# Optimization experiments

Measured on AMD Instinct MI355X. Metric: run time of the kernel, lower is better.

## Reference

```python
import jax, jax.numpy as jnp
import numpy as np
from jax import lax

KSIZE = 11
SIGMA_COLOR = 0.05
SIGMA_SPACE = 8.0
WEIGHT = (10.0, 35.0, 1.0, 10.0)

# --- fixed kernels (numpy, baked as constants) ---
_SOBEL_X = np.array([[-1, 0, 1], [-2, 0, 2], [-1, 0, 1]], np.float32).reshape(1, 1, 3, 3)
_SOBEL_Y = np.array([[1, 2, 1], [0, 0, 0], [-1, -2, -1]], np.float32).reshape(1, 1, 3, 3)

def _gaussian_window(size=11, sigma=1.5):
    g = np.exp(-((np.arange(size) - size // 2) ** 2) / (2.0 * sigma ** 2))
    g = g / g.sum()
    w = np.outer(g, g).astype(np.float32)
    return w.reshape(1, 1, size, size)

_SSIM_WIN = _gaussian_window()

# spatial weights for bilateral filter: gaussian over offset distance
_off = np.arange(KSIZE) - KSIZE // 2
_dy, _dx = np.meshgrid(_off, _off, indexing='ij')
_W_SPACE = np.exp(-(_dx ** 2 + _dy ** 2) / (2.0 * SIGMA_SPACE ** 2)).astype(np.float32).reshape(KSIZE * KSIZE, 1, 1)

def _conv2d(x, k, padding):
    return lax.conv_general_dilated(x, jnp.asarray(k), (1, 1), padding,
                                    dimension_numbers=('NCHW', 'OIHW', 'NCHW'))

def sobelxy(x):
    # ReflectionPad2d(1) then 3x3 sobel convs, |gx| + |gy|
    xp = jnp.pad(x, ((0, 0), (0, 0), (1, 1), (1, 1)), mode='reflect')
    gx = _conv2d(xp, _SOBEL_X, 'VALID')
    gy = _conv2d(xp, _SOBEL_Y, 'VALID')
    return jnp.abs(gx) + jnp.abs(gy)

def bilateral_filter(x):
    # x: [B,1,H,W]; reflect-pad, extract 11x11 patches, joint space*color weights
    p = KSIZE // 2
    xp = jnp.pad(x, ((0, 0), (0, 0), (p, p), (p, p)), mode='reflect')
    patches = lax.conv_general_dilated_patches(xp, (KSIZE, KSIZE), (1, 1), 'VALID',
                                               dimension_numbers=('NCHW', 'OIHW', 'NCHW'))
    # patches: [B, 121, H, W]; center pixel is x itself
    w_color = jnp.exp(-((patches - x) ** 2) / (2.0 * SIGMA_COLOR ** 2))
    w = w_color * jnp.asarray(_W_SPACE)[None]
    return (w * patches).sum(axis=1, keepdims=True) / w.sum(axis=1, keepdims=True)

def ssim(img1, img2):
    # standard pytorch-ssim: 11x11 gaussian window, zero-pad SAME, size_average mean
    C1, C2 = 0.01 ** 2, 0.03 ** 2
    pad = [(5, 5), (5, 5)]
    mu1 = _conv2d(img1, _SSIM_WIN, pad)
    mu2 = _conv2d(img2, _SSIM_WIN, pad)
    mu1_sq, mu2_sq, mu1_mu2 = mu1 * mu1, mu2 * mu2, mu1 * mu2
    sigma1_sq = _conv2d(img1 * img1, _SSIM_WIN, pad) - mu1_sq
    sigma2_sq = _conv2d(img2 * img2, _SSIM_WIN, pad) - mu2_sq
    sigma12 = _conv2d(img1 * img2, _SSIM_WIN, pad) - mu1_mu2
    ssim_map = ((2 * mu1_mu2 + C1) * (2 * sigma12 + C2)) / ((mu1_sq + mu2_sq + C1) * (sigma1_sq + sigma2_sq + C2))
    return ssim_map.mean()

def setup_inputs() -> dict:
    key = jax.random.key(0)
    k1, k2, k3 = jax.random.split(key, 3)
    B, H, W = 4, 480, 640
    return {
        'image_vis': jax.random.uniform(k1, (B, 3, H, W), jnp.float32),
        'image_ir': jax.random.uniform(k2, (B, 1, H, W), jnp.float32),
        'generate_img': jax.random.uniform(k3, (B, 1, H, W), jnp.float32),
    }

def reference(image_vis, image_ir, generate_img):
    image_y = image_vis[:, :1, :, :]
    x_in_max = jnp.maximum(image_y, image_ir)
    loss_in = jnp.abs(generate_img - x_in_max).mean()

    ir_grad = sobelxy(bilateral_filter(image_ir))
    y_grad = sobelxy(image_y)
    gen_grad = sobelxy(generate_img)
    x_grad_joint = jnp.maximum(y_grad, ir_grad)
    loss_grad = jnp.abs(gen_grad - x_grad_joint).mean()

    loss_tra = jnp.abs(generate_img - (image_ir + image_y) * 0.5).mean()

    loss_ssim = (1.0 - ssim(image_y, generate_img)) / 2 + (1.0 - ssim(image_ir, generate_img)) / 2

    loss_total = (WEIGHT[0] * loss_in + WEIGHT[1] * loss_grad
                  + WEIGHT[2] * loss_ssim + WEIGHT[3] * loss_tra)
    return (loss_total, loss_in, loss_grad, loss_ssim, loss_tra)
```

## Files before the change

kernel.cpp:

```cpp
#include <hip/hip_runtime.h>

#define IMG_H 480
#define IMG_W 640
#define IMG_B 4
#define HWSZ (IMG_H*IMG_W)
#define NPIX (IMG_B*HWSZ)
#define NBLK 4800

typedef float __attribute__((ext_vector_type(2))) f32x2;

constexpr float GW[11] = {
    0.00102838f, 0.00759878f, 0.03600077f, 0.10936067f, 0.21300555f,
    0.26601174f,
    0.21300555f, 0.10936067f, 0.03600077f, 0.00759878f, 0.00102838f};

constexpr float LG2WS[11] = {
    -0.28177637f, -0.18033688f, -0.10143950f, -0.04508422f, -0.01127106f,
    0.0f,
    -0.01127106f, -0.04508422f, -0.10143950f, -0.18033688f, -0.28177637f};
#define C_COLOR (-288.53900818f)

__device__ inline float fexp2(float x) {
#if __has_builtin(__builtin_amdgcn_exp2f)
    return __builtin_amdgcn_exp2f(x);
#else
    return exp2f(x);
#endif
}

__device__ inline int refl(int i, int n) {
    return i < 0 ? -i : (i >= n ? 2*n - 2 - i : i);
}

__device__ inline float sobel_abs(const float* __restrict__ p,
                                  int ym, int y0, int yp, int xm, int x0, int xp) {
    float a = p[ym*IMG_W+xm], b = p[ym*IMG_W+x0], c = p[ym*IMG_W+xp];
    float d = p[y0*IMG_W+xm],                      e = p[y0*IMG_W+xp];
    float f = p[yp*IMG_W+xm], g = p[yp*IMG_W+x0], h = p[yp*IMG_W+xp];
    float gx = (c + 2.f*e + h) - (a + 2.f*d + f);
    float gy = (a + 2.f*b + c) - (f + 2.f*g + h);
    return fabsf(gx) + fabsf(gy);
}

__global__ __launch_bounds__(256)
void bilateral_kernel(const float* __restrict__ ir, float* __restrict__ bf) {
    __shared__ __attribute__((aligned(16))) float tile[26][42];
    const int tx = threadIdx.x, ty = threadIdx.y;
    const int x0 = blockIdx.x*32, y0 = blockIdx.y*16, b = blockIdx.z;
    const float* src = ir + b*HWSZ;
    const int tid = ty*16 + tx;
    for (int i = tid; i < 26*42; i += 256) {
        int r = i / 42, c = i % 42;
        int gy = refl(y0 - 5 + r, IMG_H);
        int gx = refl(x0 - 5 + c, IMG_W);
        tile[r][c] = src[gy*IMG_W + gx];
    }
    __syncthreads();

    const int px = 2*tx;
    f32x2 cen = { tile[ty+5][px+5], tile[ty+5][px+6] };
    f32x2 num = {0.f, 0.f}, den = {0.f, 0.f};
    #pragma unroll
    for (int dy = 0; dy < 11; ++dy) {
        float w[12];
        #pragma unroll
        for (int k = 0; k < 6; ++k) {
            f32x2 p = *reinterpret_cast<const f32x2*>(&tile[ty+dy][px + 2*k]);
            w[2*k] = p.x; w[2*k+1] = p.y;
        }
        #pragma unroll
        for (int dx = 0; dx < 11; ++dx) {
            const float c2 = LG2WS[dy] + LG2WS[dx];
            f32x2 v = { w[dx], w[dx+1] };
            f32x2 d = v - cen;
            f32x2 arg = d*d*C_COLOR + c2;
            f32x2 wt;
            wt.x = fexp2(arg.x);
            wt.y = fexp2(arg.y);
            num += wt*v;
            den += wt;
        }
    }
    f32x2 res = num / den;
    *reinterpret_cast<f32x2*>(&bf[b*HWSZ + (y0+ty)*IMG_W + x0 + px]) = res;
}

__global__ __launch_bounds__(128)
void ssim_kernel(const float* __restrict__ vis, const float* __restrict__ ir,
                 const float* __restrict__ gen, float* __restrict__ parts) {
    __shared__ __attribute__((aligned(16))) float sy[18][42], si[18][42], sg[18][42];
    __shared__ __attribute__((aligned(16))) float hs[8][18][32];
    const int tx = threadIdx.x, ty = threadIdx.y;
    const int x0 = blockIdx.x*32, y0 = blockIdx.y*8, b = blockIdx.z;
    const int tid = ty*16 + tx;
    const int gid = blockIdx.x + 20*blockIdx.y + 1200*blockIdx.z;
    const float* py = vis + b*3*HWSZ;
    const float* pi = ir  + b*HWSZ;
    const float* pg = gen + b*HWSZ;

    for (int i = tid; i < 42*18; i += 128) {
        int r = i / 42, c = i % 42;
        int gy = y0 - 5 + r, gx = x0 - 5 + c;
        bool ok = (gy >= 0) & (gy < IMG_H) & (gx >= 0) & (gx < IMG_W);
        int idx = ok ? gy*IMG_W + gx : 0;
        float vy = ok ? py[idx] : 0.f;
        float vi = ok ? pi[idx] : 0.f;
        float vg = ok ? pg[idx] : 0.f;
        sy[r][c] = vy; si[r][c] = vi; sg[r][c] = vg;
    }
    __syncthreads();

    for (int i = tid; i < 18*16; i += 128) {
        int r = i / 16, c = 2*(i % 16);
        float wy[12], wi[12], wg[12];
        #pragma unroll
        for (int k = 0; k < 6; ++k) {
            f32x2 p0 = *reinterpret_cast<const f32x2*>(&sy[r][c + 2*k]);
            f32x2 p1 = *reinterpret_cast<const f32x2*>(&si[r][c + 2*k]);
            f32x2 p2 = *reinterpret_cast<const f32x2*>(&sg[r][c + 2*k]);
            wy[2*k] = p0.x; wy[2*k+1] = p0.y;
            wi[2*k] = p1.x; wi[2*k+1] = p1.y;
            wg[2*k] = p2.x; wg[2*k+1] = p2.y;
        }
        f32x2 a0={0,0},a1={0,0},a2={0,0},a3={0,0},a4={0,0},a5={0,0},a6={0,0},a7={0,0};
        #pragma unroll
        for (int dx = 0; dx < 11; ++dx) {
            const float g = GW[dx];
            f32x2 vy = { wy[dx], wy[dx+1] };
            f32x2 vi = { wi[dx], wi[dx+1] };
            f32x2 vg = { wg[dx], wg[dx+1] };
            f32x2 gy = g*vy, gi = g*vi, gg = g*vg;
            a0 += gy;    a1 += gi;    a2 += gg;
            a3 += gy*vy; a4 += gi*vi; a5 += gg*vg;
            a6 += gy*vg; a7 += gi*vg;
        }
        *reinterpret_cast<f32x2*>(&hs[0][r][c]) = a0;
        *reinterpret_cast<f32x2*>(&hs[1][r][c]) = a1;
        *reinterpret_cast<f32x2*>(&hs[2][r][c]) = a2;
        *reinterpret_cast<f32x2*>(&hs[3][r][c]) = a3;
        *reinterpret_cast<f32x2*>(&hs[4][r][c]) = a4;
        *reinterpret_cast<f32x2*>(&hs[5][r][c]) = a5;
        *reinterpret_cast<f32x2*>(&hs[6][r][c]) = a6;
        *reinterpret_cast<f32x2*>(&hs[7][r][c]) = a7;
    }
    __syncthreads();

    const int px = 2*tx;
    f32x2 s[8];
    #pragma unroll
    for (int f = 0; f < 8; ++f) {
        f32x2 acc = {0.f, 0.f};
        #pragma unroll
        for (int dy = 0; dy < 11; ++dy)
            acc += GW[dy] * (*reinterpret_cast<const f32x2*>(&hs[f][ty+dy][px]));
        s[f] = acc;
    }
    const float C1 = 1e-4f, C2 = 9e-4f;
    f32x2 muY = s[0], muI = s[1], muG = s[2];
    f32x2 vY  = s[3] - muY*muY, vI = s[4] - muI*muI, vG = s[5] - muG*muG;
    f32x2 cYG = s[6] - muY*muG, cIG = s[7] - muI*muG;
    f32x2 ssimYG = ((2.f*muY*muG + C1)*(2.f*cYG + C2)) /
                   ((muY*muY + muG*muG + C1)*(vY + vG + C2));
    f32x2 ssimIG = ((2.f*muI*muG + C1)*(2.f*cIG + C2)) /
                   ((muI*muI + muG*muG + C1)*(vI + vG + C2));

    float v0 = ssimYG.x + ssimYG.y, v1 = ssimIG.x + ssimIG.y;
    #pragma unroll
    for (int off = 32; off > 0; off >>= 1) {
        v0 += __shfl_down(v0, off);
        v1 += __shfl_down(v1, off);
    }
    __shared__ float red[2][2];
    int lane = tid & 63, wv = tid >> 6;
    if (lane == 0) { red[0][wv] = v0; red[1][wv] = v1; }
    __syncthreads();
    if (tid == 0) {
        parts[3*NBLK + gid] = red[0][0] + red[0][1];
        parts[4*NBLK + gid] = red[1][0] + red[1][1];
    }
}

__global__ __launch_bounds__(256)
void grad_kernel(const float* __restrict__ vis, const float* __restrict__ ir,
                 const float* __restrict__ gen, const float* __restrict__ bf,
                 float* __restrict__ parts) {
    const int idx = blockIdx.x*256 + threadIdx.x;
    const int b = idx / HWSZ, rem = idx % HWSZ;
    const int y = rem / IMG_W, x = rem % IMG_W;
    const float* py = vis + b*3*HWSZ;
    const float* pi = ir  + b*HWSZ;
    const float* pg = gen + b*HWSZ;
    const float* pb = bf  + b*HWSZ;

    const int ym = (y == 0) ? 1 : y-1, yp = (y == IMG_H-1) ? IMG_H-2 : y+1;
    const int xm = (x == 0) ? 1 : x-1, xp = (x == IMG_W-1) ? IMG_W-2 : x+1;

    float yg = sobel_abs(py, ym, y, yp, xm, x, xp);
    float ig = sobel_abs(pb, ym, y, yp, xm, x, xp);
    float gg = sobel_abs(pg, ym, y, yp, xm, x, xp);
    float tgrad = fabsf(gg - fmaxf(yg, ig));

    float cy = py[y*IMG_W+x], ci = pi[y*IMG_W+x], cg = pg[y*IMG_W+x];
    float tin  = fabsf(cg - fmaxf(cy, ci));
    float ttra = fabsf(cg - 0.5f*(ci + cy));

    float v0 = tin, v1 = tgrad, v2 = ttra;
    #pragma unroll
    for (int off = 32; off > 0; off >>= 1) {
        v0 += __shfl_down(v0, off);
        v1 += __shfl_down(v1, off);
        v2 += __shfl_down(v2, off);
    }
    __shared__ float red[3][4];
    int lane = threadIdx.x & 63, wv = threadIdx.x >> 6;
    if (lane == 0) { red[0][wv] = v0; red[1][wv] = v1; red[2][wv] = v2; }
    __syncthreads();
    if (threadIdx.x == 0) {
        parts[0*NBLK + blockIdx.x] = red[0][0]+red[0][1]+red[0][2]+red[0][3];
        parts[1*NBLK + blockIdx.x] = red[1][0]+red[1][1]+red[1][2]+red[1][3];
        parts[2*NBLK + blockIdx.x] = red[2][0]+red[2][1]+red[2][2]+red[2][3];
    }
}

__global__ __launch_bounds__(256)
void finalize_kernel(const float* __restrict__ parts, float* __restrict__ out) {
    const int tid = threadIdx.x;
    float s0=0,s1=0,s2=0,s3=0,s4=0;
    for (int i = tid; i < NBLK; i += 256) {
        s0 += parts[0*NBLK + i];
        s1 += parts[1*NBLK + i];
        s2 += parts[2*NBLK + i];
        s3 += parts[3*NBLK + i];
        s4 += parts[4*NBLK + i];
    }
    #pragma unroll
    for (int off = 32; off > 0; off >>= 1) {
        s0 += __shfl_down(s0, off);
        s1 += __shfl_down(s1, off);
        s2 += __shfl_down(s2, off);
        s3 += __shfl_down(s3, off);
        s4 += __shfl_down(s4, off);
    }
    __shared__ float red[5][4];
    int lane = tid & 63, wv = tid >> 6;
    if (lane == 0) { red[0][wv]=s0; red[1][wv]=s1; red[2][wv]=s2; red[3][wv]=s3; red[4][wv]=s4; }
    __syncthreads();
    if (tid == 0) {
        const float inv = 1.0f / (float)NPIX;
        float lin   = (red[0][0]+red[0][1]+red[0][2]+red[0][3]) * inv;
        float lgrad = (red[1][0]+red[1][1]+red[1][2]+red[1][3]) * inv;
        float ltra  = (red[2][0]+red[2][1]+red[2][2]+red[2][3]) * inv;
        float ssim1 = (red[3][0]+red[3][1]+red[3][2]+red[3][3]) * inv;
        float ssim2 = (red[4][0]+red[4][1]+red[4][2]+red[4][3]) * inv;
        float lssim = (1.f - ssim1)*0.5f + (1.f - ssim2)*0.5f;
        float ltot  = 10.f*lin + 35.f*lgrad + 1.f*lssim + 10.f*ltra;
        out[0] = ltot; out[1] = lin; out[2] = lgrad; out[3] = lssim; out[4] = ltra;
    }
}

extern "C" void kernel_launch(void* const* d_in, const int* in_sizes, int n_in,
                              void* d_out, int out_size, void* d_ws, size_t ws_size,
                              hipStream_t stream) {
    const float* vis = (const float*)d_in[0];
    const float* ir  = (const float*)d_in[1];
    const float* gen = (const float*)d_in[2];
    float* out = (float*)d_out;

    float* bf    = (float*)d_ws;
    float* parts = (float*)((char*)d_ws + (size_t)NPIX*4);

    dim3 blkB(16, 16);
    dim3 grdB(IMG_W/32, IMG_H/16, IMG_B);
    bilateral_kernel<<<grdB, blkB, 0, stream>>>(ir, bf);

    dim3 blkS(16, 8);
    dim3 grdS(IMG_W/32, IMG_H/8, IMG_B);
    ssim_kernel<<<grdS, blkS, 0, stream>>>(vis, ir, gen, parts);
    grad_kernel<<<NBLK, 256, 0, stream>>>(vis, ir, gen, bf, parts);
    finalize_kernel<<<1, 256, 0, stream>>>(parts, out);
}
```

Before: 144.1 us.

## Fuse gradient and intensity losses into SSIM kernel, drop separate grad pass

Merges the Sobel gradient, intensity and transfer loss terms into the SSIM kernel, so each thread also computes two horizontal pixels' Sobel gradients from global loads and all five partial sums are reduced together. This removes one kernel launch and the second full read of the vis, ir and gen images. It also pads the horizontal-pass shared buffer row to 34 floats, presumably to cut bank conflicts. The cost is more registers and global loads per SSIM thread, which may lower occupancy. The Sobel neighbours are read directly from global memory rather than from the shared tiles.

Result: faster. 139.6 us (-3.1%).

```diff
diff --git a/kernel.cpp b/kernel.cpp
--- a/kernel.cpp
+++ b/kernel.cpp
@@ -32,14 +32,16 @@
     return i < 0 ? -i : (i >= n ? 2*n - 2 - i : i);
 }
 
-__device__ inline float sobel_abs(const float* __restrict__ p,
-                                  int ym, int y0, int yp, int xm, int x0, int xp) {
-    float a = p[ym*IMG_W+xm], b = p[ym*IMG_W+x0], c = p[ym*IMG_W+xp];
-    float d = p[y0*IMG_W+xm],                      e = p[y0*IMG_W+xp];
-    float f = p[yp*IMG_W+xm], g = p[yp*IMG_W+x0], h = p[yp*IMG_W+xp];
-    float gx = (c + 2.f*e + h) - (a + 2.f*d + f);
-    float gy = (a + 2.f*b + c) - (f + 2.f*g + h);
-    return fabsf(gx) + fabsf(gy);
+__device__ inline f32x2 sobel_pair(const float m[3][4]) {
+    f32x2 gx, gy;
+    gx.x = (m[0][2] + 2.f*m[1][2] + m[2][2]) - (m[0][0] + 2.f*m[1][0] + m[2][0]);
+    gx.y = (m[0][3] + 2.f*m[1][3] + m[2][3]) - (m[0][1] + 2.f*m[1][1] + m[2][1]);
+    gy.x = (m[0][0] + 2.f*m[0][1] + m[0][2]) - (m[2][0] + 2.f*m[2][1] + m[2][2]);
+    gy.y = (m[0][1] + 2.f*m[0][2] + m[0][3]) - (m[2][1] + 2.f*m[2][2] + m[2][3]);
+    f32x2 r;
+    r.x = fabsf(gx.x) + fabsf(gy.x);
+    r.y = fabsf(gx.y) + fabsf(gy.y);
+    return r;
 }
 
 __global__ __launch_bounds__(256)
@@ -86,10 +88,11 @@
 }
 
 __global__ __launch_bounds__(128)
-void ssim_kernel(const float* __restrict__ vis, const float* __restrict__ ir,
-                 const float* __restrict__ gen, float* __restrict__ parts) {
+void fused_kernel(const float* __restrict__ vis, const float* __restrict__ ir,
+                  const float* __restrict__ gen, const float* __restrict__ bf,
+                  float* __restrict__ parts) {
     __shared__ __attribute__((aligned(16))) float sy[18][42], si[18][42], sg[18][42];
-    __shared__ __attribute__((aligned(16))) float hs[8][18][32];
+    __shared__ __attribute__((aligned(16))) float hs[8][18][34];
     const int tx = threadIdx.x, ty = threadIdx.y;
     const int x0 = blockIdx.x*32, y0 = blockIdx.y*8, b = blockIdx.z;
     const int tid = ty*16 + tx;
@@ -97,16 +100,16 @@
     const float* py = vis + b*3*HWSZ;
     const float* pi = ir  + b*HWSZ;
     const float* pg = gen + b*HWSZ;
+    const float* pb = bf  + b*HWSZ;
 
     for (int i = tid; i < 42*18; i += 128) {
         int r = i / 42, c = i % 42;
         int gy = y0 - 5 + r, gx = x0 - 5 + c;
         bool ok = (gy >= 0) & (gy < IMG_H) & (gx >= 0) & (gx < IMG_W);
         int idx = ok ? gy*IMG_W + gx : 0;
-        float vy = ok ? py[idx] : 0.f;
-        float vi = ok ? pi[idx] : 0.f;
-        float vg = ok ? pg[idx] : 0.f;
-        sy[r][c] = vy; si[r][c] = vi; sg[r][c] = vg;
+        sy[r][c] = ok ? py[idx] : 0.f;
+        si[r][c] = ok ? pi[idx] : 0.f;
+        sg[r][c] = ok ? pg[idx] : 0.f;
     }
     __syncthreads();
 
@@ -164,61 +167,60 @@
     f32x2 ssimIG = ((2.f*muI*muG + C1)*(2.f*cIG + C2)) /
                    ((muI*muI + muG*muG + C1)*(vI + vG + C2));
 
-    float v0 = ssimYG.x + ssimYG.y, v1 = ssimIG.x + ssimIG.y;
-    #pragma unroll
-    for (int off = 32; off > 0; off >>= 1) {
-        v0 += __shfl_down(v0, off);
-        v1 += __shfl_down(v1, off);
-    }
-    __shared__ float red[2][2];
-    int lane = tid & 63, wv = tid >> 6;
-    if (lane == 0) { red[0][wv] = v0; red[1][wv] = v1; }
-    __syncthreads();
-    if (tid == 0) {
-        parts[3*NBLK + gid] = red[0][0] + red[0][1];
-        parts[4*NBLK + gid] = red[1][0] + red[1][1];
-    }
-}
-
-__global__ __launch_bounds__(256)
-void grad_kernel(const float* __restrict__ vis, const float* __restrict__ ir,
-                 const float* __restrict__ gen, const float* __restrict__ bf,
-                 float* __restrict__ parts) {
-    const int idx = blockIdx.x*256 + threadIdx.x;
-    const int b = idx / HWSZ, rem = idx % HWSZ;
-    const int y = rem / IMG_W, x = rem % IMG_W;
-    const float* py = vis + b*3*HWSZ;
-    const float* pi = ir  + b*HWSZ;
-    const float* pg = gen + b*HWSZ;
-    const float* pb = bf  + b*HWSZ;
-
-    const int ym = (y == 0) ? 1 : y-1, yp = (y == IMG_H-1) ? IMG_H-2 : y+1;
-    const int xm = (x == 0) ? 1 : x-1, xp = (x == IMG_W-1) ? IMG_W-2 : x+1;
-
-    float yg = sobel_abs(py, ym, y, yp, xm, x, xp);
-    float ig = sobel_abs(pb, ym, y, yp, xm, x, xp);
-    float gg = sobel_abs(pg, ym, y, yp, xm, x, xp);
-    float tgrad = fabsf(gg - fmaxf(yg, ig));
-
-    float cy = py[y*IMG_W+x], ci = pi[y*IMG_W+x], cg = pg[y*IMG_W+x];
-    float tin  = fabsf(cg - fmaxf(cy, ci));
-    float ttra = fabsf(cg - 0.5f*(ci + cy));
-
-    float v0 = tin, v1 = tgrad, v2 = ttra;
+    const int gxx = x0 + px, gyy = y0 + ty;
+    const int xs0 = refl(gxx-1, IMG_W), xs3 = refl(gxx+2, IMG_W);
+    const int ys0 = refl(gyy-1, IMG_H), ys2 = refl(gyy+1, IMG_H);
+    const int xc[4] = {xs0, gxx, gxx+1, xs3};
+    const int yr[3] = {ys0, gyy, ys2};
+    float Ym[3][4], Gm[3][4], Bm[3][4];
+    #pragma unroll
+    for (int r = 0; r < 3; ++r) {
+        const int ro = yr[r]*IMG_W;
+        #pragma unroll
+        for (int c = 0; c < 4; ++c) {
+            Ym[r][c] = py[ro + xc[c]];
+            Gm[r][c] = pg[ro + xc[c]];
+            Bm[r][c] = pb[ro + xc[c]];
+        }
+    }
+    f32x2 ygr = sobel_pair(Ym);
+    f32x2 ggr = sobel_pair(Gm);
+    f32x2 igr = sobel_pair(Bm);
+    f32x2 jg; jg.x = fmaxf(ygr.x, igr.x); jg.y = fmaxf(ygr.y, igr.y);
+    f32x2 tgrad; tgrad.x = fabsf(ggr.x - jg.x); tgrad.y = fabsf(ggr.y - jg.y);
+
+    f32x2 cy = { Ym[1][1], Ym[1][2] };
+    f32x2 cg = { Gm[1][1], Gm[1][2] };
+    f32x2 ci = { pi[gyy*IMG_W + gxx], pi[gyy*IMG_W + gxx + 1] };
+    f32x2 tin, ttra;
+    tin.x  = fabsf(cg.x - fmaxf(cy.x, ci.x));
+    tin.y  = fabsf(cg.y - fmaxf(cy.y, ci.y));
+    ttra.x = fabsf(cg.x - 0.5f*(ci.x + cy.x));
+    ttra.y = fabsf(cg.y - 0.5f*(ci.y + cy.y));
+
+    float v0 = tin.x + tin.y;
+    float v1 = tgrad.x + tgrad.y;
+    float v2 = ttra.x + ttra.y;
+    float v3 = ssimYG.x + ssimYG.y;
+    float v4 = ssimIG.x + ssimIG.y;
     #pragma unroll
     for (int off = 32; off > 0; off >>= 1) {
         v0 += __shfl_down(v0, off);
         v1 += __shfl_down(v1, off);
         v2 += __shfl_down(v2, off);
-    }
-    __shared__ float red[3][4];
-    int lane = threadIdx.x & 63, wv = threadIdx.x >> 6;
-    if (lane == 0) { red[0][wv] = v0; red[1][wv] = v1; red[2][wv] = v2; }
-    __syncthreads();
-    if (threadIdx.x == 0) {
-        parts[0*NBLK + blockIdx.x] = red[0][0]+red[0][1]+red[0][2]+red[0][3];
-        parts[1*NBLK + blockIdx.x] = red[1][0]+red[1][1]+red[1][2]+red[1][3];
-        parts[2*NBLK + blockIdx.x] = red[2][0]+red[2][1]+red[2][2]+red[2][3];
+        v3 += __shfl_down(v3, off);
+        v4 += __shfl_down(v4, off);
+    }
+    __shared__ float red[5][2];
+    int lane = tid & 63, wv = tid >> 6;
+    if (lane == 0) { red[0][wv]=v0; red[1][wv]=v1; red[2][wv]=v2; red[3][wv]=v3; red[4][wv]=v4; }
+    __syncthreads();
+    if (tid == 0) {
+        parts[0*NBLK + gid] = red[0][0] + red[0][1];
+        parts[1*NBLK + gid] = red[1][0] + red[1][1];
+        parts[2*NBLK + gid] = red[2][0] + red[2][1];
+        parts[3*NBLK + gid] = red[3][0] + red[3][1];
+        parts[4*NBLK + gid] = red[4][0] + red[4][1];
     }
 }
 
@@ -273,9 +275,8 @@
     dim3 grdB(IMG_W/32, IMG_H/16, IMG_B);
     bilateral_kernel<<<grdB, blkB, 0, stream>>>(ir, bf);
 
-    dim3 blkS(16, 8);
-    dim3 grdS(IMG_W/32, IMG_H/8, IMG_B);
-    ssim_kernel<<<grdS, blkS, 0, stream>>>(vis, ir, gen, parts);
-    grad_kernel<<<NBLK, 256, 0, stream>>>(vis, ir, gen, bf, parts);
+    dim3 blkF(16, 8);
+    dim3 grdF(IMG_W/32, IMG_H/8, IMG_B);
+    fused_kernel<<<grdF, blkF, 0, stream>>>(vis, ir, gen, bf, parts);
     finalize_kernel<<<1, 256, 0, stream>>>(parts, out);
 }
```
